# Performance work log

Measured on AMD Instinct MI355X. Metric: run time of the kernel, lower is better.

Reference implementation:

```python
import jax, jax.numpy as jnp
import numpy as np

B, S = 2, 2048                 # batch, prefill seq len
H, HKV, D = 32, 8, 128          # num_heads, num_kv_heads, head_size
G = H // HKV                    # queries per kv head (GQA)
BLOCK_SIZE, NUM_BLOCKS = 128, 128
SCALE = 1.0 / (D ** 0.5)
NEG_INF = -1e9


def setup_inputs() -> dict:
    key = jax.random.key(0)
    kq, kk, kv, kc = jax.random.split(key, 4)
    query = jax.random.normal(kq, (B, S, H * D), dtype=jnp.float32)
    key_t = jax.random.normal(kk, (B, S, HKV * D), dtype=jnp.float32)
    value = jax.random.normal(kv, (B, S, HKV * D), dtype=jnp.float32)
    kv_cache = jax.random.normal(kc, (2, NUM_BLOCKS, BLOCK_SIZE, HKV, D), dtype=jnp.float32)
    tok = jnp.arange(B * S)
    block_indices = (tok // BLOCK_SIZE).astype(jnp.int32)   # in [0, NUM_BLOCKS)
    block_offsets = (tok % BLOCK_SIZE).astype(jnp.int32)    # in [0, BLOCK_SIZE)
    causal = jnp.tril(jnp.ones((S, S), dtype=bool))
    attn_bias = jnp.where(causal, 0.0, NEG_INF).astype(jnp.float32)[None, None]  # [1,1,S,S]
    return {"query": query, "key": key_t, "value": value, "kv_cache": kv_cache,
            "block_indices": block_indices, "block_offsets": block_offsets,
            "attn_bias": attn_bias}


def reference(query, key, value, kv_cache, block_indices, block_offsets, attn_bias):
    # --- KV cache scatter write (VLLMKVCache insert) ---
    k_tok = key.reshape(-1, HKV, D)     # [num_tokens, HKV, D]
    v_tok = value.reshape(-1, HKV, D)
    key_cache = kv_cache[0].at[block_indices, block_offsets].set(k_tok)
    value_cache = kv_cache[1].at[block_indices, block_offsets].set(v_tok)

    # --- prefill attention (xops.prompt_attention with GQA) ---
    q = query.reshape(B, S, HKV, G, D)            # split heads into kv groups
    kh = key.reshape(B, S, HKV, D)
    vh = value.reshape(B, S, HKV, D)
    scores = jnp.einsum('bqhgd,bkhd->bhgqk', q, kh) * SCALE  # [B,HKV,G,S,S]
    scores = scores + attn_bias[:, :, None]                   # bias broadcast over h,g
    probs = jax.nn.softmax(scores, axis=-1)
    out = jnp.einsum('bhgqk,bkhd->bqhgd', probs, vh)          # [B,S,HKV,G,D]
    output = out.reshape(B, S, H * D)
    return output, key_cache, value_cache
```

## Files before the change

kernel.cpp:

```cpp
#include <hip/hip_runtime.h>
#include <hip/hip_bf16.h>
#include <stdint.h>

#define B_ 2
#define S_ 2048
#define HKV_ 8
#define D_ 128

#define KVB 32
#define KTILE_SH 4096
#define VTILE_SH 4096
#define LDSBUF 16384
#define PLANE4 4194304

typedef __attribute__((ext_vector_type(8))) short bf16x8;
typedef __attribute__((ext_vector_type(16))) float f32x16;
typedef __attribute__((ext_vector_type(4))) int int4v;

typedef const __attribute__((address_space(1))) void gv_t;
typedef __attribute__((address_space(3))) void lv_t;

__device__ __forceinline__ unsigned pk2(float lo, float hi) {
  unsigned r;
  asm("v_cvt_pk_bf16_f32 %0, %1, %2" : "=v"(r) : "v"(lo), "v"(hi));
  return r;
}
__device__ __forceinline__ void plswap(unsigned& a, unsigned& b) {
  asm volatile("v_permlane32_swap_b32 %0, %1" : "+v"(a), "+v"(b));
}
__device__ __forceinline__ bf16x8 frag4(unsigned a, unsigned b, unsigned c, unsigned d) {
  union { int4v i; bf16x8 v; } u;
  u.i = int4v{(int)a, (int)b, (int)c, (int)d};
  return u.v;
}


__global__ __launch_bounds__(256)
void copy_kernel(const int4v* __restrict__ src, int4v* __restrict__ dst) {
  const int i = blockIdx.x * 256 + threadIdx.x;
#pragma unroll
  for (int j = 0; j < 16; ++j) {
    int64_t idx = (int64_t)j * 524288 + i;
    __builtin_nontemporal_store(src[idx], &dst[idx]);
  }
}


__global__ __launch_bounds__(256)
void prep_kernel(const float* __restrict__ K, const float* __restrict__ V,
                 const int* __restrict__ bi, const int* __restrict__ bo,
                 float* __restrict__ kc, float* __restrict__ vc,
                 short* __restrict__ kimg, short* __restrict__ vimg) {
  __shared__ float Vf[KVB * 132];
  const int bid = blockIdx.x;
  const int hg  = bid & 15;
  const int kt  = bid >> 4;
  const int kvh = hg & 7;
  const int b   = hg >> 3;
  const int tid = threadIdx.x;
  const int kv0 = kt * KVB;
  const float* kb = K + (int64_t)b * S_ * 1024 + kvh * 128;
  const float* vb = V + (int64_t)b * S_ * 1024 + kvh * 128;
  short* kimg_t = kimg + (int64_t)(hg * 64 + kt) * KTILE_SH;
  short* vimg_t = vimg + (int64_t)(hg * 64 + kt) * VTILE_SH;
#pragma unroll
  for (int i = 0; i < 4; ++i) {
    int idx = i * 256 + tid;
    int key = idx >> 5;
    int d0  = (idx & 31) * 4;
    int64_t roff = (int64_t)(kv0 + key) * 1024 + d0;
    float4 kf = *(const float4*)(kb + roff);
    float4 vf = *(const float4*)(vb + roff);
    int tok = b * S_ + kv0 + key;
    int64_t slot = (int64_t)bi[tok] * 128 + bo[tok];
    *(float4*)(kc + slot * 1024 + kvh * 128 + d0) = kf;
    *(float4*)(vc + slot * 1024 + kvh * 128 + d0) = vf;
    unsigned k01 = pk2(kf.x, kf.y), k23 = pk2(kf.z, kf.w);
    int koff = (d0 >> 3) * 256 + key * 8 + (d0 & 7);
    int2 st; st.x = (int)k01; st.y = (int)k23;
    *(int2*)(kimg_t + koff) = st;
    *(float4*)(&Vf[key * 132 + d0]) = vf;
  }
  __syncthreads();
  const int d  = tid & 127;
  const int kg = tid >> 7;
  const int k0 = kg * 16;
  unsigned uu[8];
#pragma unroll
  for (int i2 = 0; i2 < 8; ++i2)
    uu[i2] = pk2(Vf[(k0 + 2 * i2) * 132 + d], Vf[(k0 + 2 * i2 + 1) * 132 + d]);
  int vbase = ((d >> 5) * 4 + (k0 >> 4) * 2) * 256 + (d & 31) * 8;
  *(int4v*)(vimg_t + vbase)       = int4v{(int)uu[0], (int)uu[1], (int)uu[2], (int)uu[3]};
  *(int4v*)(vimg_t + vbase + 256) = int4v{(int)uu[4], (int)uu[5], (int)uu[6], (int)uu[7]};
}


__global__ __launch_bounds__(256, 3)
void attn_kernel(const float* __restrict__ Q, const short* __restrict__ kimg,
                 const short* __restrict__ vimg, float* __restrict__ O) {
  __shared__ int4v ldsv[2 * LDSBUF / 16];
  char* ldsb = (char*)ldsv;

  const int bid = blockIdx.x;
  const int tid = threadIdx.x;
  const int hg  = bid & 15;
  const int cc  = 63 - (bid >> 4);
  const int kvh = hg & 7;
  const int b   = hg >> 3;

  const int w   = tid >> 6;
  const int l   = tid & 63;
  const int c31 = l & 31;
  const int hi  = l >> 5;
  const int qi  = c31 & 15;
  const int hh  = c31 >> 4;
  const int qoff = cc * 32 + (w & 1) * 16;
  const int qrow = qoff + qi;
  const int h    = kvh * 4 + (w >> 1) * 2 + hh;

  const float qscale = 0.08838834764831845f * 1.4426950408889634f;

  const float* qp = Q + ((int64_t)(b * S_ + qrow)) * 4096 + h * 128;
  bf16x8 qf[8];
#pragma unroll
  for (int ks = 0; ks < 8; ++ks) {
    int d0 = ks * 16 + hi * 8;
    float4 x = *(const float4*)(qp + d0);
    float4 y = *(const float4*)(qp + d0 + 4);
    qf[ks] = frag4(pk2(x.x * qscale, x.y * qscale), pk2(x.z * qscale, x.w * qscale),
                   pk2(y.x * qscale, y.y * qscale), pk2(y.z * qscale, y.w * qscale));
  }

  f32x16 acc[4];
#pragma unroll
  for (int dt = 0; dt < 4; ++dt)
#pragma unroll
    for (int r = 0; r < 16; ++r) acc[dt][r] = 0.f;
  float m = 0.f, lsum = 0.f;

  const int nkt = cc + 1;
  const short* kimg_b = kimg + (int64_t)(hg * 64) * KTILE_SH;
  const short* vimg_b = vimg + (int64_t)(hg * 64) * VTILE_SH;

#define STAGE(KT, BUF)                                                           \
  do {                                                                           \
    const short* kg_ = kimg_b + (int64_t)(KT) * KTILE_SH;                        \
    const short* vg_ = vimg_b + (int64_t)(KT) * VTILE_SH;                        \
    char* kd_ = ldsb + (BUF) * LDSBUF;                                           \
    char* vd_ = kd_ + 8192;                                                      \
    _Pragma("unroll")                                                            \
    for (int i_ = 0; i_ < 2; ++i_) {                                             \
      int u_ = i_ * 256 + w * 64;                                                \
      __builtin_amdgcn_global_load_lds((gv_t*)(const void*)(kg_ + (u_ + l) * 8), \
                                       (lv_t*)(void*)(kd_ + u_ * 16), 16, 0, 0); \
      __builtin_amdgcn_global_load_lds((gv_t*)(const void*)(vg_ + (u_ + l) * 8), \
                                       (lv_t*)(void*)(vd_ + u_ * 16), 16, 0, 0); \
    }                                                                            \
  } while (0)

  STAGE(0, 0);

  for (int kt = 0; kt < nkt; ++kt) {
    __syncthreads();
    const int cur = kt & 1;
    if (kt + 1 < nkt) STAGE(kt + 1, cur ^ 1);
    const char* kfr = ldsb + cur * LDSBUF + hi * 512 + c31 * 16;
    const char* vfr = kfr + 8192;
    const int kv0 = kt * KVB;

    const float negm = -m;
    f32x16 s;
#pragma unroll
    for (int r = 0; r < 16; ++r) s[r] = negm;
#pragma unroll
    for (int ks = 0; ks < 8; ++ks) {
      bf16x8 kf = *(const bf16x8*)(kfr + ks * 1024);
      s = __builtin_amdgcn_mfma_f32_32x32x16_bf16(kf, qf[ks], s, 0, 0, 0);
    }

    if (kv0 + 31 > qoff) {
#pragma unroll
      for (int r = 0; r < 16; ++r) {
        int key = kv0 + (r & 3) + 8 * (r >> 2) + 4 * hi;
        if (key > qrow) s[r] = -1e30f;
      }
    }

    float a0 = fmaxf(s[0], s[1]),   a1 = fmaxf(s[2], s[3]);
    float a2 = fmaxf(s[4], s[5]),   a3 = fmaxf(s[6], s[7]);
    float a4 = fmaxf(s[8], s[9]),   a5 = fmaxf(s[10], s[11]);
    float a6 = fmaxf(s[12], s[13]), a7 = fmaxf(s[14], s[15]);
    a0 = fmaxf(a0, a1); a2 = fmaxf(a2, a3); a4 = fmaxf(a4, a5); a6 = fmaxf(a6, a7);
    float qm = fmaxf(fmaxf(a0, a2), fmaxf(a4, a6));
    qm = fmaxf(qm, __shfl_xor(qm, 32));
    if (__any(qm > 11.0f)) {
      float dsh = fmaxf(qm, 0.f);
      float al = exp2f(-dsh);
      m += dsh; lsum *= al;
#pragma unroll
      for (int r = 0; r < 16; ++r) s[r] -= dsh;
#pragma unroll
      for (int dt = 0; dt < 4; ++dt)
#pragma unroll
        for (int r = 0; r < 16; ++r) acc[dt][r] *= al;
    }
    float p[16];
#pragma unroll
    for (int r = 0; r < 16; ++r) p[r] = exp2f(s[r]);
    float b0 = (p[0] + p[1]) + (p[2] + p[3]);
    float b1 = (p[4] + p[5]) + (p[6] + p[7]);
    float b2 = (p[8] + p[9]) + (p[10] + p[11]);
    float b3 = (p[12] + p[13]) + (p[14] + p[15]);
    lsum += (b0 + b1) + (b2 + b3);

    unsigned u0 = pk2(p[0], p[1]),   u1 = pk2(p[2], p[3]);
    unsigned u2 = pk2(p[4], p[5]),   u3 = pk2(p[6], p[7]);
    unsigned u4 = pk2(p[8], p[9]),   u5 = pk2(p[10], p[11]);
    unsigned u6 = pk2(p[12], p[13]), u7 = pk2(p[14], p[15]);
    plswap(u0, u2); plswap(u1, u3);
    plswap(u4, u6); plswap(u5, u7);
    bf16x8 pf0 = frag4(u0, u1, u2, u3);
    bf16x8 pf1 = frag4(u4, u5, u6, u7);

#pragma unroll
    for (int ks2 = 0; ks2 < 2; ++ks2) {
      bf16x8 pf = ks2 ? pf1 : pf0;
#pragma unroll
      for (int dt = 0; dt < 4; ++dt) {
        bf16x8 vf = *(const bf16x8*)(vfr + (dt * 2 + ks2) * 1024);
        acc[dt] = __builtin_amdgcn_mfma_f32_32x32x16_bf16(vf, pf, acc[dt], 0, 0, 0);
      }
    }
  }
#undef STAGE

  float lt = lsum + __shfl_xor(lsum, 32);
  float inv = 1.0f / lt;
  __syncthreads();
  float* scr = (float*)ldsb + w * (32 * 33);
  float* ob = O + (int64_t)(b * S_) * 4096;
#pragma unroll
  for (int dt = 0; dt < 4; ++dt) {
#pragma unroll
    for (int r = 0; r < 16; ++r) {
      int crow = (r & 3) + 8 * (r >> 2) + 4 * hi;
      scr[c31 * 33 + crow] = acc[dt][r] * inv;
    }
    asm volatile("" ::: "memory");
#pragma unroll
    for (int rr = 0; rr < 16; ++rr) {
      int col = rr * 2 + hi;
      float val = scr[col * 33 + c31];
      int qi2 = col & 15, hh2 = col >> 4;
      int qq = cc * 32 + (w & 1) * 16 + qi2;
      int h2 = kvh * 4 + (w >> 1) * 2 + hh2;
      ob[(int64_t)qq * 4096 + h2 * 128 + dt * 32 + c31] = val;
    }
    asm volatile("" ::: "memory");
  }
}

extern "C" void kernel_launch(void* const* d_in, const int* in_sizes, int n_in,
                              void* d_out, int out_size, void* d_ws, size_t ws_size,
                              hipStream_t stream) {
  const float* Q   = (const float*)d_in[0];
  const float* K   = (const float*)d_in[1];
  const float* V   = (const float*)d_in[2];
  const float* kvc = (const float*)d_in[3];
  const int*   bi  = (const int*)d_in[4];
  const int*   bo  = (const int*)d_in[5];

  float* out = (float*)d_out;
  float* kc = out + (int64_t)B_ * S_ * 32 * 128;
  float* vc = kc + (int64_t)128 * 128 * HKV_ * D_;

  short* kimg = (short*)d_ws;
  short* vimg = kimg + (int64_t)1024 * KTILE_SH;

  hipLaunchKernelGGL(copy_kernel, dim3(2048), dim3(256), 0, stream,
                     (const int4v*)kvc, (int4v*)kc);
  hipLaunchKernelGGL(prep_kernel, dim3(1024), dim3(256), 0, stream,
                     K, V, bi, bo, kc, vc, kimg, vimg);
  hipLaunchKernelGGL(attn_kernel, dim3(1024), dim3(256), 0, stream,
                     Q, kimg, vimg, out);
}
```

Measured before the change: 182.8 us.

## Merge copy into prep kernel, move cache scatter into attention, triple-buffer LDS

The cache copy and the K/V bf16 image prep now run in one launch, which removes a kernel boundary. The scatter of new K/V tokens into the cache moves to extra blocks appended to the attention grid, so that memory-bound work overlaps the compute-bound attention blocks. The attention loop goes from double to triple buffering, waiting with explicit vmcnt and a raw barrier so loads can run two tiles ahead. The cost is 48KB of LDS per block, which may lower occupancy below the requested three blocks per CU. The cache copy to kc must also finish before the scatter writes to kc, and stream order between the two launches provides that.

After: 175.0 us. 1.04x faster.

```diff
diff --git a/kernel.cpp b/kernel.cpp
--- a/kernel.cpp
+++ b/kernel.cpp
@@ -11,7 +11,10 @@
 #define KTILE_SH 4096
 #define VTILE_SH 4096
 #define LDSBUF 16384
-#define PLANE4 4194304
+#define NATTN 1024
+#define NSCAT 256
+#define NPREP 1024
+#define NCOPY 2048
 
 typedef __attribute__((ext_vector_type(8))) short bf16x8;
 typedef __attribute__((ext_vector_type(16))) float f32x16;
@@ -36,28 +39,27 @@
 
 
 __global__ __launch_bounds__(256)
-void copy_kernel(const int4v* __restrict__ src, int4v* __restrict__ dst) {
-  const int i = blockIdx.x * 256 + threadIdx.x;
-#pragma unroll
-  for (int j = 0; j < 16; ++j) {
-    int64_t idx = (int64_t)j * 524288 + i;
-    __builtin_nontemporal_store(src[idx], &dst[idx]);
-  }
-}
-
-
-__global__ __launch_bounds__(256)
-void prep_kernel(const float* __restrict__ K, const float* __restrict__ V,
-                 const int* __restrict__ bi, const int* __restrict__ bo,
-                 float* __restrict__ kc, float* __restrict__ vc,
-                 short* __restrict__ kimg, short* __restrict__ vimg) {
+void prepcopy_kernel(const float* __restrict__ K, const float* __restrict__ V,
+                     short* __restrict__ kimg, short* __restrict__ vimg,
+                     const int4v* __restrict__ kvc, int4v* __restrict__ cdst) {
   __shared__ float Vf[KVB * 132];
   const int bid = blockIdx.x;
+  const int tid = threadIdx.x;
+
+  if (bid >= NPREP) {
+    const int i = (bid - NPREP) * 256 + tid;
+#pragma unroll
+    for (int j = 0; j < 16; ++j) {
+      int64_t idx = (int64_t)j * 524288 + i;
+      __builtin_nontemporal_store(kvc[idx], &cdst[idx]);
+    }
+    return;
+  }
+
   const int hg  = bid & 15;
   const int kt  = bid >> 4;
   const int kvh = hg & 7;
   const int b   = hg >> 3;
-  const int tid = threadIdx.x;
   const int kv0 = kt * KVB;
   const float* kb = K + (int64_t)b * S_ * 1024 + kvh * 128;
   const float* vb = V + (int64_t)b * S_ * 1024 + kvh * 128;
@@ -71,10 +73,6 @@
     int64_t roff = (int64_t)(kv0 + key) * 1024 + d0;
     float4 kf = *(const float4*)(kb + roff);
     float4 vf = *(const float4*)(vb + roff);
-    int tok = b * S_ + kv0 + key;
-    int64_t slot = (int64_t)bi[tok] * 128 + bo[tok];
-    *(float4*)(kc + slot * 1024 + kvh * 128 + d0) = kf;
-    *(float4*)(vc + slot * 1024 + kvh * 128 + d0) = vf;
     unsigned k01 = pk2(kf.x, kf.y), k23 = pk2(kf.z, kf.w);
     int koff = (d0 >> 3) * 256 + key * 8 + (d0 & 7);
     int2 st; st.x = (int)k01; st.y = (int)k23;
@@ -97,12 +95,30 @@
 
 __global__ __launch_bounds__(256, 3)
 void attn_kernel(const float* __restrict__ Q, const short* __restrict__ kimg,
-                 const short* __restrict__ vimg, float* __restrict__ O) {
-  __shared__ int4v ldsv[2 * LDSBUF / 16];
+                 const short* __restrict__ vimg, float* __restrict__ O,
+                 const int4v* __restrict__ key4, const int4v* __restrict__ val4,
+                 const int* __restrict__ bi, const int* __restrict__ bo,
+                 int4v* __restrict__ kc4, int4v* __restrict__ vc4) {
+  __shared__ int4v ldsv[3 * LDSBUF / 16];
   char* ldsb = (char*)ldsv;
 
   const int bid = blockIdx.x;
   const int tid = threadIdx.x;
+
+  if (bid >= NATTN) {
+    const int base = (bid - NATTN) * 256 + tid;
+#pragma unroll
+    for (int i = 0; i < 16; ++i) {
+      int idx = base + i * 65536;
+      int t = idx >> 8;
+      int rem = idx & 255;
+      int64_t slot = (int64_t)bi[t] * 128 + bo[t];
+      kc4[slot * 256 + rem] = key4[(int64_t)t * 256 + rem];
+      vc4[slot * 256 + rem] = val4[(int64_t)t * 256 + rem];
+    }
+    return;
+  }
+
   const int hg  = bid & 15;
   const int cc  = 63 - (bid >> 4);
   const int kvh = hg & 7;
@@ -159,12 +175,15 @@
   } while (0)
 
   STAGE(0, 0);
+  if (nkt > 1) STAGE(1, 1);
 
   for (int kt = 0; kt < nkt; ++kt) {
-    __syncthreads();
-    const int cur = kt & 1;
-    if (kt + 1 < nkt) STAGE(kt + 1, cur ^ 1);
-    const char* kfr = ldsb + cur * LDSBUF + hi * 512 + c31 * 16;
+    if (kt + 1 < nkt) asm volatile("s_waitcnt vmcnt(4)" ::: "memory");
+    else              asm volatile("s_waitcnt vmcnt(0)" ::: "memory");
+    __builtin_amdgcn_s_barrier();
+    asm volatile("" ::: "memory");
+    if (kt + 2 < nkt) STAGE(kt + 2, (kt + 2) % 3);
+    const char* kfr = ldsb + (kt % 3) * LDSBUF + hi * 512 + c31 * 16;
     const char* vfr = kfr + 8192;
     const int kv0 = kt * KVB;
 
@@ -277,10 +296,10 @@
   short* kimg = (short*)d_ws;
   short* vimg = kimg + (int64_t)1024 * KTILE_SH;
 
-  hipLaunchKernelGGL(copy_kernel, dim3(2048), dim3(256), 0, stream,
-                     (const int4v*)kvc, (int4v*)kc);
-  hipLaunchKernelGGL(prep_kernel, dim3(1024), dim3(256), 0, stream,
-                     K, V, bi, bo, kc, vc, kimg, vimg);
-  hipLaunchKernelGGL(attn_kernel, dim3(1024), dim3(256), 0, stream,
-                     Q, kimg, vimg, out);
-}
+  hipLaunchKernelGGL(prepcopy_kernel, dim3(NPREP + NCOPY), dim3(256), 0, stream,
+                     K, V, kimg, vimg, (const int4v*)kvc, (int4v*)kc);
+  hipLaunchKernelGGL(attn_kernel, dim3(NATTN + NSCAT), dim3(256), 0, stream,
+                     Q, kimg, vimg, out,
+                     (const int4v*)K, (const int4v*)V, bi, bo,
+                     (int4v*)kc, (int4v*)vc);
+}
```
